# Kernel optimization log

Measured on AMD Instinct MI355X. Metric: run time of the kernel, lower is better.

Reference implementation:

```python
import jax, jax.numpy as jnp
import numpy as np

N, E, G = 100000, 400000, 2000   # nodes, edges, graphs
IN, H = 48, 128                  # in_channels, hidden_channels (= out_channels)
L = 6                            # num GIN layers
EPS = 1e-5                       # BatchNorm eps
SLOPE = 0.01                     # leaky_relu negative slope


def setup_inputs() -> dict:
    key = jax.random.key(0)
    ks = jax.random.split(key, 12)
    x = jax.random.normal(ks[0], (N, IN), jnp.float32)
    edge_index = jax.random.randint(ks[1], (2, E), 0, N)
    edge_attr = jax.random.normal(ks[2], (E, 4), jnp.float32)  # ignored by GINConv
    # sorted graph-assignment vector; guarantee every graph has >=1 node
    batch = jnp.sort(jnp.concatenate([jnp.arange(G),
                                      jax.random.randint(ks[3], (N - G,), 0, G)]))
    s = 0.05
    W1a = jax.random.normal(ks[4], (IN, H), jnp.float32) * s        # layer-0 MLP lin1
    W1b = jax.random.normal(ks[5], (L - 1, H, H), jnp.float32) * s  # layers 1..5 MLP lin1
    b1 = jnp.zeros((L, H), jnp.float32)
    g1 = jnp.ones((L, H), jnp.float32)    # inner BN scale
    be1 = jnp.zeros((L, H), jnp.float32)  # inner BN bias
    W2 = jax.random.normal(ks[6], (L, H, H), jnp.float32) * s       # MLP lin2
    b2 = jnp.zeros((L, H), jnp.float32)
    gn = jnp.ones((L - 1, H), jnp.float32)    # outer BN scale (layers 0..4)
    bn_b = jnp.zeros((L - 1, H), jnp.float32) # outer BN bias
    fc_w = jax.random.normal(ks[7], (2 * H, 64), jnp.float32) * s
    fc_b = jnp.zeros((64,), jnp.float32)
    fc2_w = jax.random.normal(ks[8], (64, 3), jnp.float32) * s
    fc2_b = jnp.zeros((3,), jnp.float32)
    return dict(x=x, edge_attr=edge_attr, W1a=W1a, W1b=W1b, b1=b1, g1=g1, be1=be1,
                W2=W2, b2=b2, gn=gn, bn_b=bn_b, fc_w=fc_w, fc_b=fc_b,
                fc2_w=fc2_w, fc2_b=fc2_b, edge_index=edge_index, batch=batch,
                num_graphs=G)


def _bn(h, g, b):
    # training-mode BatchNorm1d over node dim (biased variance, as torch)
    m = jnp.mean(h, axis=0)
    v = jnp.mean((h - m) ** 2, axis=0)
    return g * (h - m) * jax.lax.rsqrt(v + EPS) + b


def _lrelu(h):
    return jnp.where(h >= 0, h, SLOPE * h)


def reference(x, edge_attr, W1a, W1b, b1, g1, be1, W2, b2, gn, bn_b,
              fc_w, fc_b, fc2_w, fc2_b, edge_index, batch, num_graphs):
    del edge_attr  # GINConv does not use edge attributes
    src, dst = edge_index[0], edge_index[1]
    n = x.shape[0]
    h = x
    for l in range(L):
        # GINConv: (1 + eps) * x + sum_{j in N(i)} x_j, eps = 0
        agg = jax.ops.segment_sum(h[src], dst, num_segments=n)
        z = h + agg
        W1 = W1a if l == 0 else W1b[l - 1]
        # MLP([in, H, H]) with inner BatchNorm + leaky_relu, plain last linear
        z = _lrelu(_bn(z @ W1 + b1[l], g1[l], be1[l])) @ W2[l] + b2[l]
        if l < L - 1:  # outer norm + act, skipped on last layer
            z = _lrelu(_bn(z, gn[l], bn_b[l]))
        h = z
    # dual global pooling over ragged per-graph segments
    cnt = jax.ops.segment_sum(jnp.ones((n, 1), h.dtype), batch, num_segments=num_graphs)
    p1 = jax.ops.segment_sum(h, batch, num_segments=num_graphs) / jnp.maximum(cnt, 1.0)
    p2 = jax.ops.segment_max(h, batch, num_segments=num_graphs)
    emb = jnp.concatenate([p1, p2], axis=1)            # [G, 256]
    out = _lrelu(emb @ fc_w + fc_b) @ fc2_w + fc2_b    # [G, 3]
    return out, emb
```

## Files before the change

### kernel.cpp

```cpp
#include <hip/hip_runtime.h>
#include <stdint.h>

#define N_NODES 100000
#define N_EDGES 400000
#define N_GRAPHS 2000
#define C_IN 48
#define HD 128
#define NLAYERS 6
#define BN_EPS 1e-5f
#define NSLOPE 0.01f
#define SB 391
#define NREP 8

typedef uint16_t u16;
typedef uint32_t u32;
typedef short bf16x8 __attribute__((ext_vector_type(8)));
typedef float f32x4 __attribute__((ext_vector_type(4)));

__device__ __forceinline__ float bf2f_lo(u32 v) { return __uint_as_float(v << 16); }
__device__ __forceinline__ float bf2f_hi(u32 v) { return __uint_as_float(v & 0xffff0000u); }
__device__ __forceinline__ float bf2f(u16 h) { return __uint_as_float(((u32)h) << 16); }
__device__ __forceinline__ u16 f2bf(float f) {
    u32 u = __float_as_uint(f);
    u32 r = (u + 0x7fffu + ((u >> 16) & 1u)) >> 16;
    return (u16)r;
}
__device__ __forceinline__ u32 pack2(float a, float b) {
    return (u32)f2bf(a) | ((u32)f2bf(b) << 16);
}
__device__ __forceinline__ float lrelu(float v) { return v >= 0.f ? v : v * NSLOPE; }

__global__ __launch_bounds__(256) void detect_kernel(const u16* __restrict__ x, int* __restrict__ mode) {
    __shared__ int flag;
    if (threadIdx.x == 0) flag = 0;
    __syncthreads();
    int local = 0;
    for (int i = threadIdx.x; i < 16384; i += 256) {
        float a = fabsf(bf2f(x[i]));
        if (!(a < 1e4f)) local = 1;
    }
    if (local) flag = 1;
    __syncthreads();
    if (threadIdx.x == 0) mode[0] = flag;
}

__global__ __launch_bounds__(256) void hist_kernel(const int* __restrict__ dst, int* __restrict__ cnt) {
    int e = blockIdx.x * 256 + threadIdx.x;
    if (e < N_EDGES) atomicAdd(&cnt[dst[e]], 1);
}

__global__ __launch_bounds__(256) void scan1_kernel(const int* __restrict__ cnt, int* __restrict__ bsum) {
    __shared__ int s[256];
    const int t = threadIdx.x;
    const int i = blockIdx.x * 256 + t;
    s[t] = (i < N_NODES) ? cnt[i] : 0;
    __syncthreads();
    for (int d = 128; d > 0; d >>= 1) {
        if (t < d) s[t] += s[t + d];
        __syncthreads();
    }
    if (t == 0) bsum[blockIdx.x] = s[0];
}

__global__ __launch_bounds__(512) void scan2_kernel(int* __restrict__ bsum, int* __restrict__ row_ptr) {
    __shared__ int s[SB];
    const int t = threadIdx.x;
    if (t < SB) s[t] = bsum[t];
    __syncthreads();
    if (t == 0) {
        int run = 0;
        for (int b = 0; b < SB; ++b) { int v = s[b]; s[b] = run; run += v; }
        row_ptr[0] = 0;
    }
    __syncthreads();
    if (t < SB) bsum[t] = s[t];
}

__global__ __launch_bounds__(256) void scan3_kernel(const int* __restrict__ cnt, const int* __restrict__ bsum,
                                                    int* __restrict__ row_ptr) {
    __shared__ int s[256];
    const int t = threadIdx.x;
    const int i = blockIdx.x * 256 + t;
    s[t] = (i < N_NODES) ? cnt[i] : 0;
    __syncthreads();
    if (t == 0) {
        int run = bsum[blockIdx.x];
        for (int j = 0; j < 256; ++j) { run += s[j]; s[j] = run; }
    }
    __syncthreads();
    if (i < N_NODES) row_ptr[i + 1] = s[t];
}

__global__ __launch_bounds__(256) void fill_kernel(const int* __restrict__ src, const int* __restrict__ dst,
                                                   int* __restrict__ cursor, int* __restrict__ col_idx) {
    int e = blockIdx.x * 256 + threadIdx.x;
    if (e < N_EDGES) {
        int d = dst[e];
        int slot = atomicAdd(&cursor[d], 1);
        col_idx[slot] = src[e];
    }
}

__global__ __launch_bounds__(256) void pack_w_kernel(const void* __restrict__ W1a, const void* __restrict__ W1b,
                                                     const void* __restrict__ W2, const int* __restrict__ mode,
                                                     u16* __restrict__ wpack) {
    const int t = blockIdx.x * 256 + threadIdx.x;
    if (t >= 24576) return;
    const int mat = t >> 11;
    const int r = t & 2047;
    const int l = r & 63;
    const int f = r >> 6;
    const int kb = f >> 3, nt = f & 7;
    const int k0 = kb * 32 + (l >> 4) * 8;
    const int n = nt * 16 + (l & 15);
    const int md = *mode;
    u16 vals[8];
    #pragma unroll
    for (int j = 0; j < 8; ++j) {
        const int k = k0 + j;
        float v;
        if (mat == 0) {
            v = (k < C_IN) ? (md ? ((const float*)W1a)[k * HD + n] : bf2f(((const u16*)W1a)[k * HD + n])) : 0.f;
        } else if (mat < 6) {
            const size_t o = (size_t)(mat - 1) * HD * HD + (size_t)k * HD + n;
            v = md ? ((const float*)W1b)[o] : bf2f(((const u16*)W1b)[o]);
        } else {
            const size_t o = (size_t)(mat - 6) * HD * HD + (size_t)k * HD + n;
            v = md ? ((const float*)W2)[o] : bf2f(((const u16*)W2)[o]);
        }
        vals[j] = f2bf(v);
    }
    uint4 o;
    o.x = (u32)vals[0] | ((u32)vals[1] << 16);
    o.y = (u32)vals[2] | ((u32)vals[3] << 16);
    o.z = (u32)vals[4] | ((u32)vals[5] << 16);
    o.w = (u32)vals[6] | ((u32)vals[7] << 16);
    *reinterpret_cast<uint4*>(wpack + (size_t)t * 8) = o;
}

__global__ __launch_bounds__(256) void pack_b_kernel(const void* __restrict__ b1, const void* __restrict__ b2,
                                                     const int* __restrict__ mode, float* __restrict__ biasf) {
    const int i = blockIdx.x * 256 + threadIdx.x;
    if (i >= 12 * HD) return;
    const int mat = i >> 7, c = i & 127;
    const int md = *mode;
    float v;
    if (mat < 6) v = md ? ((const float*)b1)[mat * HD + c] : bf2f(((const u16*)b1)[mat * HD + c]);
    else         v = md ? ((const float*)b2)[(mat - 6) * HD + c] : bf2f(((const u16*)b2)[(mat - 6) * HD + c]);
    biasf[i] = v;
}

__device__ __forceinline__ void coef_to_lds(float* coefs, const float* __restrict__ instats,
                                            const void* __restrict__ gammav, const void* __restrict__ betav,
                                            size_t gelem, int md, int tid) {
    if (tid < 128) {
        float sm = 0.f, sq = 0.f;
        #pragma unroll
        for (int rep = 0; rep < NREP; ++rep) {
            sm += instats[rep * 256 + tid];
            sq += instats[rep * 256 + 128 + tid];
        }
        const float inv_n = 1.0f / (float)N_NODES;
        const float mean = sm * inv_n;
        const float var = fmaxf(sq * inv_n - mean * mean, 0.f);
        const float rs = rsqrtf(var + BN_EPS);
        const float g  = md ? ((const float*)gammav)[gelem + tid] : bf2f(((const u16*)gammav)[gelem + tid]);
        const float be = md ? ((const float*)betav)[gelem + tid]  : bf2f(((const u16*)betav)[gelem + tid]);
        const float A = g * rs;
        coefs[tid] = A;
        coefs[128 + tid] = be - A * mean;
    }
}

template <int TRANS, int STATS>
__global__ __launch_bounds__(256) void gemm_mfma(const u16* A, const u16* __restrict__ wp,
                                                 const float* __restrict__ biasf,
                                                 const float* __restrict__ instats,
                                                 const void* __restrict__ gammav, const void* __restrict__ betav,
                                                 size_t gelem, const int* __restrict__ mode,
                                                 u16* out, float* __restrict__ stats) {
    __shared__ u16 Asm[32][136];
    __shared__ float sred[2][128];
    __shared__ float sqred[2][128];
    __shared__ float coefs[256];
    const int tid = threadIdx.x;
    const int m0 = blockIdx.x * 32;
    const int rrow = tid >> 4;
    const int seg = tid & 15;

    if (TRANS) {
        coef_to_lds(coefs, instats, gammav, betav, gelem, *mode, tid);
        __syncthreads();
    }

    {
        float cA[8], cB[8];
        if (TRANS) {
            #pragma unroll
            for (int j = 0; j < 8; ++j) {
                cA[j] = coefs[seg * 8 + j];
                cB[j] = coefs[128 + seg * 8 + j];
            }
        }
        uint4 v[2];
        #pragma unroll
        for (int i = 0; i < 2; ++i) {
            const int gm = m0 + i * 16 + rrow;
            if (gm < N_NODES) v[i] = *reinterpret_cast<const uint4*>(A + (size_t)gm * HD + seg * 8);
            else { v[i].x = 0; v[i].y = 0; v[i].z = 0; v[i].w = 0; }
        }
        #pragma unroll
        for (int i = 0; i < 2; ++i) {
            uint4 o = v[i];
            if (TRANS) {
                u32 w[4] = {o.x, o.y, o.z, o.w};
                #pragma unroll
                for (int p = 0; p < 4; ++p) {
                    const float lo = lrelu(cA[2 * p] * bf2f_lo(w[p]) + cB[2 * p]);
                    const float hi = lrelu(cA[2 * p + 1] * bf2f_hi(w[p]) + cB[2 * p + 1]);
                    w[p] = pack2(lo, hi);
                }
                o.x = w[0]; o.y = w[1]; o.z = w[2]; o.w = w[3];
            }
            *reinterpret_cast<uint4*>(&Asm[i * 16 + rrow][seg * 8]) = o;
        }
    }
    __syncthreads();

    const int wave = tid >> 6, lane = tid & 63;
    const int quad = lane >> 4, lx = lane & 15;
    const int rowhalf = wave & 1;
    const int colhalf = wave >> 1;
    const int wrow = rowhalf * 16;
    f32x4 acc[4] = {};
    #pragma unroll
    for (int kb = 0; kb < 4; ++kb) {
        bf16x8 bfr[4];
        #pragma unroll
        for (int nt = 0; nt < 4; ++nt)
            bfr[nt] = *reinterpret_cast<const bf16x8*>(wp + (((size_t)(kb * 8 + colhalf * 4 + nt) * 64 + lane) << 3));
        const bf16x8 af = *reinterpret_cast<const bf16x8*>(&Asm[wrow + lx][kb * 32 + quad * 8]);
        #pragma unroll
        for (int nt = 0; nt < 4; ++nt)
            acc[nt] = __builtin_amdgcn_mfma_f32_16x16x32_bf16(af, bfr[nt], acc[nt], 0, 0, 0);
    }

    const int mrow0 = m0 + wrow;
    #pragma unroll
    for (int nt = 0; nt < 4; ++nt) {
        const int n = colhalf * 64 + nt * 16 + lx;
        const float bj = biasf[n];
        float s = 0.f, q = 0.f;
        #pragma unroll
        for (int r = 0; r < 4; ++r) {
            const int m = mrow0 + quad * 4 + r;
            if (m < N_NODES) {
                const float v = acc[nt][r] + bj;
                out[(size_t)m * HD + n] = f2bf(v);
                if (STATS) { s += v; q += v * v; }
            }
        }
        if (STATS) {
            s += __shfl_xor(s, 16); s += __shfl_xor(s, 32);
            q += __shfl_xor(q, 16); q += __shfl_xor(q, 32);
            if (quad == 0) { sred[rowhalf][n] = s; sqred[rowhalf][n] = q; }
        }
    }
    if (STATS) {
        __syncthreads();
        float* sdst = stats + (size_t)(blockIdx.x & (NREP - 1)) * 256;
        if (tid < 128) {
            atomicAdd(&sdst[tid], sred[0][tid] + sred[1][tid]);
        } else if (tid < 256) {
            const int c2 = tid - 128;
            atomicAdd(&sdst[128 + c2], sqred[0][c2] + sqred[1][c2]);
        }
    }
}

__global__ __launch_bounds__(256) void gemm_gather(const u16* __restrict__ U, const int* __restrict__ row_ptr,
                                                   const int* __restrict__ col_idx, const u16* __restrict__ wp,
                                                   const float* __restrict__ biasf,
                                                   const float* __restrict__ instats,
                                                   const void* __restrict__ gammav, const void* __restrict__ betav,
                                                   size_t gelem, const int* __restrict__ mode,
                                                   u16* __restrict__ out, float* __restrict__ stats) {
    __shared__ u16 Asm[16][136];
    __shared__ float sred[128];
    __shared__ float sqred[128];
    __shared__ float coefs[256];
    const int tid = threadIdx.x;
    const int m0 = blockIdx.x * 16;
    const int rrow = tid >> 4;
    const int seg = tid & 15;

    coef_to_lds(coefs, instats, gammav, betav, gelem, *mode, tid);
    __syncthreads();

    {
        float cA[8], cB[8];
        #pragma unroll
        for (int j = 0; j < 8; ++j) {
            cA[j] = coefs[seg * 8 + j];
            cB[j] = coefs[128 + seg * 8 + j];
        }
        const int gm = m0 + rrow;
        float a[8];
        #pragma unroll
        for (int j = 0; j < 8; ++j) a[j] = 0.f;
        if (gm < N_NODES) {
            const uint4 v = *reinterpret_cast<const uint4*>(U + (size_t)gm * HD + seg * 8);
            const u32 w[4] = {v.x, v.y, v.z, v.w};
            #pragma unroll
            for (int p = 0; p < 4; ++p) {
                a[2 * p]     = lrelu(cA[2 * p] * bf2f_lo(w[p]) + cB[2 * p]);
                a[2 * p + 1] = lrelu(cA[2 * p + 1] * bf2f_hi(w[p]) + cB[2 * p + 1]);
            }
            const int s = row_ptr[gm];
            const int deg = row_ptr[gm + 1] - s;
            for (int t = 0; t < deg; t += 2) {
                const int id0 = col_idx[s + t];
                const bool h1 = (t + 1) < deg;
                const int id1 = h1 ? col_idx[s + t + 1] : 0;
                const uint4 r0 = *reinterpret_cast<const uint4*>(U + (size_t)id0 * HD + seg * 8);
                uint4 r1; r1.x = r1.y = r1.z = r1.w = 0;
                if (h1) r1 = *reinterpret_cast<const uint4*>(U + (size_t)id1 * HD + seg * 8);
                const u32 w0[4] = {r0.x, r0.y, r0.z, r0.w};
                const u32 w1[4] = {r1.x, r1.y, r1.z, r1.w};
                #pragma unroll
                for (int p = 0; p < 4; ++p) {
                    a[2 * p]     += lrelu(cA[2 * p] * bf2f_lo(w0[p]) + cB[2 * p]);
                    a[2 * p + 1] += lrelu(cA[2 * p + 1] * bf2f_hi(w0[p]) + cB[2 * p + 1]);
                    if (h1) {
                        a[2 * p]     += lrelu(cA[2 * p] * bf2f_lo(w1[p]) + cB[2 * p]);
                        a[2 * p + 1] += lrelu(cA[2 * p + 1] * bf2f_hi(w1[p]) + cB[2 * p + 1]);
                    }
                }
            }
        }
        uint4 o;
        o.x = pack2(a[0], a[1]); o.y = pack2(a[2], a[3]);
        o.z = pack2(a[4], a[5]); o.w = pack2(a[6], a[7]);
        *reinterpret_cast<uint4*>(&Asm[rrow][seg * 8]) = o;
    }
    __syncthreads();

    const int wave = tid >> 6, lane = tid & 63;
    const int quad = lane >> 4, lx = lane & 15;
    f32x4 acc[2] = {};
    #pragma unroll
    for (int kb = 0; kb < 4; ++kb) {
        bf16x8 bfr[2];
        #pragma unroll
        for (int nt = 0; nt < 2; ++nt)
            bfr[nt] = *reinterpret_cast<const bf16x8*>(wp + (((size_t)(kb * 8 + wave * 2 + nt) * 64 + lane) << 3));
        const bf16x8 af = *reinterpret_cast<const bf16x8*>(&Asm[lx][kb * 32 + quad * 8]);
        #pragma unroll
        for (int nt = 0; nt < 2; ++nt)
            acc[nt] = __builtin_amdgcn_mfma_f32_16x16x32_bf16(af, bfr[nt], acc[nt], 0, 0, 0);
    }

    #pragma unroll
    for (int nt = 0; nt < 2; ++nt) {
        const int n = wave * 32 + nt * 16 + lx;
        const float bj = biasf[n];
        float s = 0.f, q = 0.f;
        #pragma unroll
        for (int r = 0; r < 4; ++r) {
            const int m = m0 + quad * 4 + r;
            if (m < N_NODES) {
                const float v = acc[nt][r] + bj;
                out[(size_t)m * HD + n] = f2bf(v);
                s += v; q += v * v;
            }
        }
        s += __shfl_xor(s, 16); s += __shfl_xor(s, 32);
        q += __shfl_xor(q, 16); q += __shfl_xor(q, 32);
        if (quad == 0) { sred[n] = s; sqred[n] = q; }
    }
    __syncthreads();
    float* sdst = stats + (size_t)(blockIdx.x & (NREP - 1)) * 256;
    if (tid < 128) {
        atomicAdd(&sdst[tid], sred[tid]);
    } else if (tid < 256) {
        const int c2 = tid - 128;
        atomicAdd(&sdst[128 + c2], sqred[c2]);
    }
}

__global__ __launch_bounds__(256) void gemm_gather0(const void* __restrict__ xv, const int* __restrict__ row_ptr,
                                                    const int* __restrict__ col_idx, const u16* __restrict__ wp,
                                                    const float* __restrict__ biasf, const int* __restrict__ mode,
                                                    u16* __restrict__ out, float* __restrict__ stats) {
    __shared__ u16 Asm[16][136];
    __shared__ float sred[128];
    __shared__ float sqred[128];
    const int tid = threadIdx.x;
    const int m0 = blockIdx.x * 16;
    const int rrow = tid >> 4;
    const int seg = tid & 15;
    const int md = *mode;
    const bool act = seg < 6;

    {
        const int gm = m0 + rrow;
        float a[8];
        #pragma unroll
        for (int j = 0; j < 8; ++j) a[j] = 0.f;
        if (gm < N_NODES && act) {
            if (md) {
                const float* xf = (const float*)xv + (size_t)gm * C_IN + seg * 8;
                const float4 v0 = reinterpret_cast<const float4*>(xf)[0];
                const float4 v1 = reinterpret_cast<const float4*>(xf)[1];
                a[0] = v0.x; a[1] = v0.y; a[2] = v0.z; a[3] = v0.w;
                a[4] = v1.x; a[5] = v1.y; a[6] = v1.z; a[7] = v1.w;
            } else {
                const uint4 v = *reinterpret_cast<const uint4*>((const u16*)xv + (size_t)gm * C_IN + seg * 8);
                const u32 w[4] = {v.x, v.y, v.z, v.w};
                #pragma unroll
                for (int p = 0; p < 4; ++p) { a[2 * p] = bf2f_lo(w[p]); a[2 * p + 1] = bf2f_hi(w[p]); }
            }
        }
        if (gm < N_NODES) {
            const int s = row_ptr[gm];
            const int deg = row_ptr[gm + 1] - s;
            for (int t = 0; t < deg; t += 2) {
                const int id0 = col_idx[s + t];
                const bool h1 = (t + 1) < deg;
                const int id1 = h1 ? col_idx[s + t + 1] : 0;
                if (act) {
                    if (md) {
                        const float* p0 = (const float*)xv + (size_t)id0 * C_IN + seg * 8;
                        const float4 u0 = reinterpret_cast<const float4*>(p0)[0];
                        const float4 u1 = reinterpret_cast<const float4*>(p0)[1];
                        a[0] += u0.x; a[1] += u0.y; a[2] += u0.z; a[3] += u0.w;
                        a[4] += u1.x; a[5] += u1.y; a[6] += u1.z; a[7] += u1.w;
                        if (h1) {
                            const float* p1 = (const float*)xv + (size_t)id1 * C_IN + seg * 8;
                            const float4 t0 = reinterpret_cast<const float4*>(p1)[0];
                            const float4 t1 = reinterpret_cast<const float4*>(p1)[1];
                            a[0] += t0.x; a[1] += t0.y; a[2] += t0.z; a[3] += t0.w;
                            a[4] += t1.x; a[5] += t1.y; a[6] += t1.z; a[7] += t1.w;
                        }
                    } else {
                        const uint4 r0 = *reinterpret_cast<const uint4*>((const u16*)xv + (size_t)id0 * C_IN + seg * 8);
                        const u32 w0[4] = {r0.x, r0.y, r0.z, r0.w};
                        #pragma unroll
                        for (int p = 0; p < 4; ++p) { a[2 * p] += bf2f_lo(w0[p]); a[2 * p + 1] += bf2f_hi(w0[p]); }
                        if (h1) {
                            const uint4 r1 = *reinterpret_cast<const uint4*>((const u16*)xv + (size_t)id1 * C_IN + seg * 8);
                            const u32 w1[4] = {r1.x, r1.y, r1.z, r1.w};
                            #pragma unroll
                            for (int p = 0; p < 4; ++p) { a[2 * p] += bf2f_lo(w1[p]); a[2 * p + 1] += bf2f_hi(w1[p]); }
                        }
                    }
                }
            }
        }
        uint4 o;
        o.x = pack2(a[0], a[1]); o.y = pack2(a[2], a[3]);
        o.z = pack2(a[4], a[5]); o.w = pack2(a[6], a[7]);
        *reinterpret_cast<uint4*>(&Asm[rrow][seg * 8]) = o;
    }
    __syncthreads();

    const int wave = tid >> 6, lane = tid & 63;
    const int quad = lane >> 4, lx = lane & 15;
    f32x4 acc[2] = {};
    #pragma unroll
    for (int kb = 0; kb < 4; ++kb) {
        bf16x8 bfr[2];
        #pragma unroll
        for (int nt = 0; nt < 2; ++nt)
            bfr[nt] = *reinterpret_cast<const bf16x8*>(wp + (((size_t)(kb * 8 + wave * 2 + nt) * 64 + lane) << 3));
        const bf16x8 af = *reinterpret_cast<const bf16x8*>(&Asm[lx][kb * 32 + quad * 8]);
        #pragma unroll
        for (int nt = 0; nt < 2; ++nt)
            acc[nt] = __builtin_amdgcn_mfma_f32_16x16x32_bf16(af, bfr[nt], acc[nt], 0, 0, 0);
    }

    #pragma unroll
    for (int nt = 0; nt < 2; ++nt) {
        const int n = wave * 32 + nt * 16 + lx;
        const float bj = biasf[n];
        float s = 0.f, q = 0.f;
        #pragma unroll
        for (int r = 0; r < 4; ++r) {
            const int m = m0 + quad * 4 + r;
            if (m < N_NODES) {
                const float v = acc[nt][r] + bj;
                out[(size_t)m * HD + n] = f2bf(v);
                s += v; q += v * v;
            }
        }
        s += __shfl_xor(s, 16); s += __shfl_xor(s, 32);
        q += __shfl_xor(q, 16); q += __shfl_xor(q, 32);
        if (quad == 0) { sred[n] = s; sqred[n] = q; }
    }
    __syncthreads();
    float* sdst = stats + (size_t)(blockIdx.x & (NREP - 1)) * 256;
    if (tid < 128) {
        atomicAdd(&sdst[tid], sred[tid]);
    } else if (tid < 256) {
        const int c2 = tid - 128;
        atomicAdd(&sdst[128 + c2], sqred[c2]);
    }
}

__global__ __launch_bounds__(256) void pool_kernel(const u16* __restrict__ hf, const int* __restrict__ batch,
                                                   const int* __restrict__ mode, float* __restrict__ emb,
                                                   void* __restrict__ outv) {
    const int wave = threadIdx.x >> 6, lane = threadIdx.x & 63;
    const int g = blockIdx.x * 4 + wave;
    if (g >= N_GRAPHS) return;
    const int md = *mode;
    const int quad = lane >> 4, c = lane & 15;
    int lo = 0, hi = N_NODES;
    while (lo < hi) { int m = (lo + hi) >> 1; if (batch[m] < g) lo = m + 1; else hi = m; }
    const int s = lo;
    hi = N_NODES;
    while (lo < hi) { int m = (lo + hi) >> 1; if (batch[m] < g + 1) lo = m + 1; else hi = m; }
    const int e = lo;
    const int cnt = e - s;
    float sum[8], mx[8];
    #pragma unroll
    for (int j = 0; j < 8; ++j) { sum[j] = 0.f; mx[j] = -INFINITY; }
    for (int n = s + quad; n < e; n += 4) {
        const uint4 v = *reinterpret_cast<const uint4*>(hf + (size_t)n * HD + c * 8);
        const u32 w[4] = {v.x, v.y, v.z, v.w};
        #pragma unroll
        for (int p = 0; p < 4; ++p) {
            const float f0 = bf2f_lo(w[p]), f1 = bf2f_hi(w[p]);
            sum[2 * p] += f0; sum[2 * p + 1] += f1;
            mx[2 * p] = fmaxf(mx[2 * p], f0); mx[2 * p + 1] = fmaxf(mx[2 * p + 1], f1);
        }
    }
    #pragma unroll
    for (int j = 0; j < 8; ++j) {
        sum[j] += __shfl_xor(sum[j], 16); sum[j] += __shfl_xor(sum[j], 32);
        mx[j] = fmaxf(mx[j], __shfl_xor(mx[j], 16));
        mx[j] = fmaxf(mx[j], __shfl_xor(mx[j], 32));
    }
    if (quad == 0) {
        const float invc = 1.0f / (float)max(cnt, 1);
        const size_t base = (size_t)N_GRAPHS * 3 + (size_t)g * 256;
        #pragma unroll
        for (int j = 0; j < 8; ++j) {
            const float mean = sum[j] * invc;
            const float m2 = (cnt == 0) ? 0.f : mx[j];
            const int col = c * 8 + j;
            emb[(size_t)g * 256 + col] = mean;
            emb[(size_t)g * 256 + 128 + col] = m2;
            if (md) {
                ((float*)outv)[base + col] = mean;
                ((float*)outv)[base + 128 + col] = m2;
            } else {
                ((u16*)outv)[base + col] = f2bf(mean);
                ((u16*)outv)[base + 128 + col] = f2bf(m2);
            }
        }
    }
}

__global__ __launch_bounds__(64) void final_kernel(const float* __restrict__ emb, const void* __restrict__ fcwv,
                                                   const void* __restrict__ fcbv, const void* __restrict__ fc2wv,
                                                   const void* __restrict__ fc2bv, const int* __restrict__ mode,
                                                   void* __restrict__ outv) {
    __shared__ float es[256];
    __shared__ float hs[64];
    const int g = blockIdx.x, t = threadIdx.x;
    const int md = *mode;
    reinterpret_cast<float4*>(es)[t] = reinterpret_cast<const float4*>(emb + (size_t)g * 256)[t];
    __syncthreads();
    float acc = md ? ((const float*)fcbv)[t] : bf2f(((const u16*)fcbv)[t]);
    if (md) {
        const float* w = (const float*)fcwv;
        #pragma unroll 8
        for (int k = 0; k < 256; ++k) acc += es[k] * w[k * 64 + t];
    } else {
        const u16* w = (const u16*)fcwv;
        #pragma unroll 8
        for (int k = 0; k < 256; ++k) acc += es[k] * bf2f(w[k * 64 + t]);
    }
    hs[t] = lrelu(acc);
    __syncthreads();
    if (t < 3) {
        float o = md ? ((const float*)fc2bv)[t] : bf2f(((const u16*)fc2bv)[t]);
        if (md) {
            const float* w = (const float*)fc2wv;
            #pragma unroll 8
            for (int j = 0; j < 64; ++j) o += hs[j] * w[j * 3 + t];
            ((float*)outv)[(size_t)g * 3 + t] = o;
        } else {
            const u16* w = (const u16*)fc2wv;
            #pragma unroll 8
            for (int j = 0; j < 64; ++j) o += hs[j] * bf2f(w[j * 3 + t]);
            ((u16*)outv)[(size_t)g * 3 + t] = f2bf(o);
        }
    }
}

static inline size_t align256(size_t x) { return (x + 255) & ~(size_t)255; }

extern "C" void kernel_launch(void* const* d_in, const int* in_sizes, int n_in,
                              void* d_out, int out_size, void* d_ws, size_t ws_size,
                              hipStream_t stream) {
    (void)in_sizes; (void)n_in; (void)out_size; (void)ws_size;
    const void* x    = d_in[0];
    const void* W1a  = d_in[2];
    const void* W1b  = d_in[3];
    const void* b1   = d_in[4];
    const void* g1   = d_in[5];
    const void* be1  = d_in[6];
    const void* W2   = d_in[7];
    const void* b2   = d_in[8];
    const void* gn   = d_in[9];
    const void* bnb  = d_in[10];
    const void* fcw  = d_in[11];
    const void* fcb  = d_in[12];
    const void* fc2w = d_in[13];
    const void* fc2b = d_in[14];
    const int* ei    = (const int*)d_in[15];
    const int* batch = (const int*)d_in[16];

    char* p = (char*)d_ws;
    size_t off = 0;
    u16* zb = (u16*)(p + off); off += align256((size_t)N_NODES * HD * 2);
    u16* hb = (u16*)(p + off); off += align256((size_t)N_NODES * HD * 2);
    u16* wpack = (u16*)(p + off); off += align256((size_t)12 * HD * HD * 2);
    float* biasf = (float*)(p + off); off += align256((size_t)12 * HD * 4);
    float* emb = (float*)(p + off); off += align256((size_t)N_GRAPHS * 256 * 4);
    int* row_ptr = (int*)(p + off); off += align256((size_t)(N_NODES + 1) * 4);
    int* cursor = (int*)(p + off); off += align256((size_t)N_NODES * 4);
    int* col_idx = (int*)(p + off); off += align256((size_t)N_EDGES * 4);
    int* bsum = (int*)(p + off); off += align256((size_t)SB * 4);
    float* statsAll = (float*)(p + off); off += align256((size_t)12 * NREP * 256 * 4);
    int* mode = (int*)(p + off); off += align256(4);

    const int EB = (N_EDGES + 255) / 256;
    const int GBM = (N_NODES + 31) / 32;
    const int GBG = (N_NODES + 15) / 16;

    detect_kernel<<<1, 256, 0, stream>>>((const u16*)x, mode);

    hipMemsetAsync(cursor, 0, (size_t)N_NODES * 4, stream);
    hipMemsetAsync(statsAll, 0, (size_t)12 * NREP * 256 * 4, stream);
    hist_kernel<<<EB, 256, 0, stream>>>(ei + N_EDGES, cursor);
    scan1_kernel<<<SB, 256, 0, stream>>>(cursor, bsum);
    scan2_kernel<<<1, 512, 0, stream>>>(bsum, row_ptr);
    scan3_kernel<<<SB, 256, 0, stream>>>(cursor, bsum, row_ptr);
    hipMemcpyAsync(cursor, row_ptr, (size_t)N_NODES * 4, hipMemcpyDeviceToDevice, stream);
    fill_kernel<<<EB, 256, 0, stream>>>(ei, ei + N_EDGES, cursor, col_idx);
    pack_w_kernel<<<96, 256, 0, stream>>>(W1a, W1b, W2, mode, wpack);
    pack_b_kernel<<<6, 256, 0, stream>>>(b1, b2, mode, biasf);

    u16* cur = zb;
    u16* oth = hb;
    for (int l = 0; l < NLAYERS; ++l) {
        float* statsA = statsAll + (size_t)l * NREP * 256;
        float* statsB = statsAll + (size_t)(6 + l) * NREP * 256;
        float* statsBprev = statsAll + (size_t)(6 + l - 1) * NREP * 256;
        if (l == 0) {
            gemm_gather0<<<GBG, 256, 0, stream>>>(x, row_ptr, col_idx, wpack,
                                                  biasf, mode, cur, statsA);
        } else {
            gemm_gather<<<GBG, 256, 0, stream>>>(cur, row_ptr, col_idx,
                                                 wpack + (size_t)l * HD * HD,
                                                 biasf + (size_t)l * HD, statsBprev, gn, bnb,
                                                 (size_t)(l - 1) * HD, mode, oth, statsA);
            u16* t = cur; cur = oth; oth = t;
        }
        if (l < NLAYERS - 1) {
            gemm_mfma<1, 1><<<GBM, 256, 0, stream>>>(cur, wpack + (size_t)(6 + l) * HD * HD,
                                                     biasf + (size_t)(6 + l) * HD, statsA, g1, be1,
                                                     (size_t)l * HD, mode, cur, statsB);
        } else {
            gemm_mfma<1, 0><<<GBM, 256, 0, stream>>>(cur, wpack + (size_t)(6 + l) * HD * HD,
                                                     biasf + (size_t)(6 + l) * HD, statsA, g1, be1,
                                                     (size_t)l * HD, mode, cur, nullptr);
        }
    }

    pool_kernel<<<(N_GRAPHS + 3) / 4, 256, 0, stream>>>(cur, batch, mode, emb, d_out);
    final_kernel<<<N_GRAPHS, 64, 0, stream>>>(emb, fcw, fcb, fc2w, fc2b, mode, d_out);
}
```

Before: 504.4 us.

## Gather neighbors edge-parallel per 32-row tile with LDS float atomics

Rewrites the fused gather+GEMM kernels so that each block handles 32 rows. The block stages that range's edge list and the row owning each edge in LDS, then spreads the neighbor row loads evenly across all threads. Partial sums go into an fp32 LDS accumulator through atomic adds, replacing the old per-row serial loop over degree. This targets load imbalance from varying node degrees and the half-width 16-row MFMA tile, at the cost of LDS atomics, more shared memory per block, and bounds checks removed on the assumption that N is divisible by 32.

New measurement: 1.773 ms. 251% more time.

```diff
diff --git a/kernel.cpp b/kernel.cpp
--- a/kernel.cpp
+++ b/kernel.cpp
@@ -11,6 +11,7 @@
 #define NSLOPE 0.01f
 #define SB 391
 #define NREP 8
+#define ECAP 1024
 
 typedef uint16_t u16;
 typedef uint32_t u32;
@@ -29,6 +30,15 @@
     return (u32)f2bf(a) | ((u32)f2bf(b) << 16);
 }
 __device__ __forceinline__ float lrelu(float v) { return v >= 0.f ? v : v * NSLOPE; }
+
+__device__ __forceinline__ void bn_store8(float* dst, const uint4 v, const float* cA, const float* cB) {
+    const u32 w[4] = {v.x, v.y, v.z, v.w};
+    #pragma unroll
+    for (int p = 0; p < 4; ++p) {
+        dst[2 * p]     = lrelu(cA[2 * p] * bf2f_lo(w[p]) + cB[2 * p]);
+        dst[2 * p + 1] = lrelu(cA[2 * p + 1] * bf2f_hi(w[p]) + cB[2 * p + 1]);
+    }
+}
 
 __global__ __launch_bounds__(256) void detect_kernel(const u16* __restrict__ x, int* __restrict__ mode) {
     __shared__ int flag;
@@ -169,6 +179,55 @@
         const float A = g * rs;
         coefs[tid] = A;
         coefs[128 + tid] = be - A * mean;
+    }
+}
+
+__device__ __forceinline__ void mfma_epilogue32(const u16 (*Asm)[136], const u16* __restrict__ wp,
+                                                const float* __restrict__ biasf,
+                                                float sred[2][128], float sqred[2][128],
+                                                int m0, int tid, int bidx,
+                                                u16* __restrict__ out, float* __restrict__ stats) {
+    const int wave = tid >> 6, lane = tid & 63;
+    const int quad = lane >> 4, lx = lane & 15;
+    const int rowhalf = wave & 1;
+    const int colhalf = wave >> 1;
+    const int wrow = rowhalf * 16;
+    f32x4 acc[4] = {};
+    #pragma unroll
+    for (int kb = 0; kb < 4; ++kb) {
+        bf16x8 bfr[4];
+        #pragma unroll
+        for (int nt = 0; nt < 4; ++nt)
+            bfr[nt] = *reinterpret_cast<const bf16x8*>(wp + (((size_t)(kb * 8 + colhalf * 4 + nt) * 64 + lane) << 3));
+        const bf16x8 af = *reinterpret_cast<const bf16x8*>(&Asm[wrow + lx][kb * 32 + quad * 8]);
+        #pragma unroll
+        for (int nt = 0; nt < 4; ++nt)
+            acc[nt] = __builtin_amdgcn_mfma_f32_16x16x32_bf16(af, bfr[nt], acc[nt], 0, 0, 0);
+    }
+    const int mrow0 = m0 + wrow;
+    #pragma unroll
+    for (int nt = 0; nt < 4; ++nt) {
+        const int n = colhalf * 64 + nt * 16 + lx;
+        const float bj = biasf[n];
+        float s = 0.f, q = 0.f;
+        #pragma unroll
+        for (int r = 0; r < 4; ++r) {
+            const int m = mrow0 + quad * 4 + r;
+            const float v = acc[nt][r] + bj;
+            out[(size_t)m * HD + n] = f2bf(v);
+            s += v; q += v * v;
+        }
+        s += __shfl_xor(s, 16); s += __shfl_xor(s, 32);
+        q += __shfl_xor(q, 16); q += __shfl_xor(q, 32);
+        if (quad == 0) { sred[rowhalf][n] = s; sqred[rowhalf][n] = q; }
+    }
+    __syncthreads();
+    float* sdst = stats + (size_t)(bidx & (NREP - 1)) * 256;
+    if (tid < 128) {
+        atomicAdd(&sdst[tid], sred[0][tid] + sred[1][tid]);
+    } else {
+        const int c2 = tid - 128;
+        atomicAdd(&sdst[128 + c2], sqred[0][c2] + sqred[1][c2]);
     }
 }
 
@@ -206,8 +265,7 @@
         #pragma unroll
         for (int i = 0; i < 2; ++i) {
             const int gm = m0 + i * 16 + rrow;
-            if (gm < N_NODES) v[i] = *reinterpret_cast<const uint4*>(A + (size_t)gm * HD + seg * 8);
-            else { v[i].x = 0; v[i].y = 0; v[i].z = 0; v[i].w = 0; }
+            v[i] = *reinterpret_cast<const uint4*>(A + (size_t)gm * HD + seg * 8);
         }
         #pragma unroll
         for (int i = 0; i < 2; ++i) {
@@ -254,11 +312,9 @@
         #pragma unroll
         for (int r = 0; r < 4; ++r) {
             const int m = mrow0 + quad * 4 + r;
-            if (m < N_NODES) {
-                const float v = acc[nt][r] + bj;
-                out[(size_t)m * HD + n] = f2bf(v);
-                if (STATS) { s += v; q += v * v; }
-            }
+            const float v = acc[nt][r] + bj;
+            out[(size_t)m * HD + n] = f2bf(v);
+            if (STATS) { s += v; q += v * v; }
         }
         if (STATS) {
             s += __shfl_xor(s, 16); s += __shfl_xor(s, 32);
@@ -271,7 +327,7 @@
         float* sdst = stats + (size_t)(blockIdx.x & (NREP - 1)) * 256;
         if (tid < 128) {
             atomicAdd(&sdst[tid], sred[0][tid] + sred[1][tid]);
-        } else if (tid < 256) {
+        } else {
             const int c2 = tid - 128;
             atomicAdd(&sdst[128 + c2], sqred[0][c2] + sqred[1][c2]);
         }
@@ -279,232 +335,196 @@
 }
 
 __global__ __launch_bounds__(256) void gemm_gather(const u16* __restrict__ U, const int* __restrict__ row_ptr,
-                                                   const int* __restrict__ col_idx, const u16* __restrict__ wp,
+                                                   const int* __restrict__ col_idx,
+                                                   const u16* __restrict__ wp,
                                                    const float* __restrict__ biasf,
                                                    const float* __restrict__ instats,
                                                    const void* __restrict__ gammav, const void* __restrict__ betav,
                                                    size_t gelem, const int* __restrict__ mode,
                                                    u16* __restrict__ out, float* __restrict__ stats) {
-    __shared__ u16 Asm[16][136];
-    __shared__ float sred[128];
-    __shared__ float sqred[128];
+    __shared__ float accf[32][132];
     __shared__ float coefs[256];
+    __shared__ int rp[33];
+    __shared__ int eidx[ECAP];
+    __shared__ u16 rowOf[ECAP];
+    __shared__ u16 Asm[32][136];
+    __shared__ float sred[2][128];
+    __shared__ float sqred[2][128];
     const int tid = threadIdx.x;
-    const int m0 = blockIdx.x * 16;
+    const int m0 = blockIdx.x * 32;
     const int rrow = tid >> 4;
     const int seg = tid & 15;
 
     coef_to_lds(coefs, instats, gammav, betav, gelem, *mode, tid);
-    __syncthreads();
+    if (tid < 33) rp[tid] = row_ptr[m0 + tid];
+    __syncthreads();
+
+    float cA[8], cB[8];
+    #pragma unroll
+    for (int j = 0; j < 8; ++j) {
+        cA[j] = coefs[seg * 8 + j];
+        cB[j] = coefs[128 + seg * 8 + j];
+    }
 
     {
-        float cA[8], cB[8];
-        #pragma unroll
-        for (int j = 0; j < 8; ++j) {
-            cA[j] = coefs[seg * 8 + j];
-            cB[j] = coefs[128 + seg * 8 + j];
-        }
-        const int gm = m0 + rrow;
-        float a[8];
-        #pragma unroll
-        for (int j = 0; j < 8; ++j) a[j] = 0.f;
-        if (gm < N_NODES) {
-            const uint4 v = *reinterpret_cast<const uint4*>(U + (size_t)gm * HD + seg * 8);
+        const uint4 v0 = *reinterpret_cast<const uint4*>(U + (size_t)(m0 + rrow) * HD + seg * 8);
+        const uint4 v1 = *reinterpret_cast<const uint4*>(U + (size_t)(m0 + 16 + rrow) * HD + seg * 8);
+        bn_store8(&accf[rrow][seg * 8], v0, cA, cB);
+        bn_store8(&accf[16 + rrow][seg * 8], v1, cA, cB);
+    }
+
+    const int e0 = rp[0], e1 = rp[32];
+    for (int base = e0; base < e1; base += ECAP) {
+        const int n = min(ECAP, e1 - base);
+        __syncthreads();
+        for (int k = tid; k < n; k += 256) {
+            const int e = base + k;
+            eidx[k] = col_idx[e];
+            int lo = 0, hi = 32;
+            #pragma unroll
+            for (int it = 0; it < 5; ++it) { const int mid = (lo + hi) >> 1; if (e >= rp[mid]) lo = mid; else hi = mid; }
+            rowOf[k] = (u16)lo;
+        }
+        __syncthreads();
+        const int items = n << 4;
+        for (int k = tid; k < items; k += 256) {
+            const int e = k >> 4;
+            const int nb = eidx[e];
+            const int r = rowOf[e];
+            const uint4 v = *reinterpret_cast<const uint4*>(U + (size_t)nb * HD + seg * 8);
             const u32 w[4] = {v.x, v.y, v.z, v.w};
+            float* arow = &accf[r][seg * 8];
             #pragma unroll
             for (int p = 0; p < 4; ++p) {
-                a[2 * p]     = lrelu(cA[2 * p] * bf2f_lo(w[p]) + cB[2 * p]);
-                a[2 * p + 1] = lrelu(cA[2 * p + 1] * bf2f_hi(w[p]) + cB[2 * p + 1]);
+                atomicAdd(&arow[2 * p],     lrelu(cA[2 * p] * bf2f_lo(w[p]) + cB[2 * p]));
+                atomicAdd(&arow[2 * p + 1], lrelu(cA[2 * p + 1] * bf2f_hi(w[p]) + cB[2 * p + 1]));
             }
-            const int s = row_ptr[gm];
-            const int deg = row_ptr[gm + 1] - s;
-            for (int t = 0; t < deg; t += 2) {
-                const int id0 = col_idx[s + t];
-                const bool h1 = (t + 1) < deg;
-                const int id1 = h1 ? col_idx[s + t + 1] : 0;
-                const uint4 r0 = *reinterpret_cast<const uint4*>(U + (size_t)id0 * HD + seg * 8);
-                uint4 r1; r1.x = r1.y = r1.z = r1.w = 0;
-                if (h1) r1 = *reinterpret_cast<const uint4*>(U + (size_t)id1 * HD + seg * 8);
-                const u32 w0[4] = {r0.x, r0.y, r0.z, r0.w};
-                const u32 w1[4] = {r1.x, r1.y, r1.z, r1.w};
-                #pragma unroll
-                for (int p = 0; p < 4; ++p) {
-                    a[2 * p]     += lrelu(cA[2 * p] * bf2f_lo(w0[p]) + cB[2 * p]);
-                    a[2 * p + 1] += lrelu(cA[2 * p + 1] * bf2f_hi(w0[p]) + cB[2 * p + 1]);
-                    if (h1) {
-                        a[2 * p]     += lrelu(cA[2 * p] * bf2f_lo(w1[p]) + cB[2 * p]);
-                        a[2 * p + 1] += lrelu(cA[2 * p + 1] * bf2f_hi(w1[p]) + cB[2 * p + 1]);
+        }
+    }
+    __syncthreads();
+
+    {
+        const float* s0 = &accf[rrow][seg * 8];
+        const float* s1 = &accf[16 + rrow][seg * 8];
+        uint4 o0, o1;
+        o0.x = pack2(s0[0], s0[1]); o0.y = pack2(s0[2], s0[3]);
+        o0.z = pack2(s0[4], s0[5]); o0.w = pack2(s0[6], s0[7]);
+        o1.x = pack2(s1[0], s1[1]); o1.y = pack2(s1[2], s1[3]);
+        o1.z = pack2(s1[4], s1[5]); o1.w = pack2(s1[6], s1[7]);
+        *reinterpret_cast<uint4*>(&Asm[rrow][seg * 8]) = o0;
+        *reinterpret_cast<uint4*>(&Asm[16 + rrow][seg * 8]) = o1;
+    }
+    __syncthreads();
+
+    mfma_epilogue32(Asm, wp, biasf, sred, sqred, m0, tid, blockIdx.x, out, stats);
+}
+
+__global__ __launch_bounds__(256) void gemm_gather0(const void* __restrict__ xv, const int* __restrict__ row_ptr,
+                                                    const int* __restrict__ col_idx,
+                                                    const u16* __restrict__ wp,
+                                                    const float* __restrict__ biasf, const int* __restrict__ mode,
+                                                    u16* __restrict__ out, float* __restrict__ stats) {
+    __shared__ float accf[32][132];
+    __shared__ int rp[33];
+    __shared__ int eidx[ECAP];
+    __shared__ u16 rowOf[ECAP];
+    __shared__ u16 Asm[32][136];
+    __shared__ float sred[2][128];
+    __shared__ float sqred[2][128];
+    const int tid = threadIdx.x;
+    const int m0 = blockIdx.x * 32;
+    const int rrow = tid >> 4;
+    const int seg = tid & 15;
+    const int md = *mode;
+
+    if (tid < 33) rp[tid] = row_ptr[m0 + tid];
+
+    if (md) {
+        if (seg < 12) {
+            const float4 v0 = *reinterpret_cast<const float4*>((const float*)xv + (size_t)(m0 + rrow) * C_IN + seg * 4);
+            const float4 v1 = *reinterpret_cast<const float4*>((const float*)xv + (size_t)(m0 + 16 + rrow) * C_IN + seg * 4);
+            float* a0 = &accf[rrow][seg * 4];
+            float* a1 = &accf[16 + rrow][seg * 4];
+            a0[0] = v0.x; a0[1] = v0.y; a0[2] = v0.z; a0[3] = v0.w;
+            a1[0] = v1.x; a1[1] = v1.y; a1[2] = v1.z; a1[3] = v1.w;
+        }
+    } else {
+        if (seg < 6) {
+            const uint4 v0 = *reinterpret_cast<const uint4*>((const u16*)xv + (size_t)(m0 + rrow) * C_IN + seg * 8);
+            const uint4 v1 = *reinterpret_cast<const uint4*>((const u16*)xv + (size_t)(m0 + 16 + rrow) * C_IN + seg * 8);
+            const u32 w0[4] = {v0.x, v0.y, v0.z, v0.w};
+            const u32 w1[4] = {v1.x, v1.y, v1.z, v1.w};
+            float* a0 = &accf[rrow][seg * 8];
+            float* a1 = &accf[16 + rrow][seg * 8];
+            #pragma unroll
+            for (int p = 0; p < 4; ++p) {
+                a0[2 * p] = bf2f_lo(w0[p]); a0[2 * p + 1] = bf2f_hi(w0[p]);
+                a1[2 * p] = bf2f_lo(w1[p]); a1[2 * p + 1] = bf2f_hi(w1[p]);
+            }
+        }
+    }
+    __syncthreads();
+
+    const int e0 = rp[0], e1 = rp[32];
+    for (int base = e0; base < e1; base += ECAP) {
+        const int n = min(ECAP, e1 - base);
+        __syncthreads();
+        for (int k = tid; k < n; k += 256) {
+            const int e = base + k;
+            eidx[k] = col_idx[e];
+            int lo = 0, hi = 32;
+            #pragma unroll
+            for (int it = 0; it < 5; ++it) { const int mid = (lo + hi) >> 1; if (e >= rp[mid]) lo = mid; else hi = mid; }
+            rowOf[k] = (u16)lo;
+        }
+        __syncthreads();
+        const int items = n << 4;
+        for (int k = tid; k < items; k += 256) {
+            const int e = k >> 4;
+            const int nb = eidx[e];
+            const int r = rowOf[e];
+            if (md) {
+                if (seg < 12) {
+                    const float4 v = *reinterpret_cast<const float4*>((const float*)xv + (size_t)nb * C_IN + seg * 4);
+                    float* arow = &accf[r][seg * 4];
+                    atomicAdd(&arow[0], v.x); atomicAdd(&arow[1], v.y);
+                    atomicAdd(&arow[2], v.z); atomicAdd(&arow[3], v.w);
+                }
+            } else {
+                if (seg < 6) {
+                    const uint4 v = *reinterpret_cast<const uint4*>((const u16*)xv + (size_t)nb * C_IN + seg * 8);
+                    const u32 w[4] = {v.x, v.y, v.z, v.w};
+                    float* arow = &accf[r][seg * 8];
+                    #pragma unroll
+                    for (int p = 0; p < 4; ++p) {
+                        atomicAdd(&arow[2 * p], bf2f_lo(w[p]));
+                        atomicAdd(&arow[2 * p + 1], bf2f_hi(w[p]));
                     }
                 }
             }
         }
-        uint4 o;
-        o.x = pack2(a[0], a[1]); o.y = pack2(a[2], a[3]);
-        o.z = pack2(a[4], a[5]); o.w = pack2(a[6], a[7]);
-        *reinterpret_cast<uint4*>(&Asm[rrow][seg * 8]) = o;
-    }
-    __syncthreads();
-
-    const int wave = tid >> 6, lane = tid & 63;
-    const int quad = lane >> 4, lx = lane & 15;
-    f32x4 acc[2] = {};
-    #pragma unroll
-    for (int kb = 0; kb < 4; ++kb) {
-        bf16x8 bfr[2];
-        #pragma unroll
-        for (int nt = 0; nt < 2; ++nt)
-            bfr[nt] = *reinterpret_cast<const bf16x8*>(wp + (((size_t)(kb * 8 + wave * 2 + nt) * 64 + lane) << 3));
-        const bf16x8 af = *reinterpret_cast<const bf16x8*>(&Asm[lx][kb * 32 + quad * 8]);
-        #pragma unroll
-        for (int nt = 0; nt < 2; ++nt)
-            acc[nt] = __builtin_amdgcn_mfma_f32_16x16x32_bf16(af, bfr[nt], acc[nt], 0, 0, 0);
-    }
-
-    #pragma unroll
-    for (int nt = 0; nt < 2; ++nt) {
-        const int n = wave * 32 + nt * 16 + lx;
-        const float bj = biasf[n];
-        float s = 0.f, q = 0.f;
-        #pragma unroll
-        for (int r = 0; r < 4; ++r) {
-            const int m = m0 + quad * 4 + r;
-            if (m < N_NODES) {
-                const float v = acc[nt][r] + bj;
-                out[(size_t)m * HD + n] = f2bf(v);
-                s += v; q += v * v;
-            }
-        }
-        s += __shfl_xor(s, 16); s += __shfl_xor(s, 32);
-        q += __shfl_xor(q, 16); q += __shfl_xor(q, 32);
-        if (quad == 0) { sred[n] = s; sqred[n] = q; }
-    }
-    __syncthreads();
-    float* sdst = stats + (size_t)(blockIdx.x & (NREP - 1)) * 256;
-    if (tid < 128) {
-        atomicAdd(&sdst[tid], sred[tid]);
-    } else if (tid < 256) {
-        const int c2 = tid - 128;
-        atomicAdd(&sdst[128 + c2], sqred[c2]);
-    }
-}
-
-__global__ __launch_bounds__(256) void gemm_gather0(const void* __restrict__ xv, const int* __restrict__ row_ptr,
-                                                    const int* __restrict__ col_idx, const u16* __restrict__ wp,
-                                                    const float* __restrict__ biasf, const int* __restrict__ mode,
-                                                    u16* __restrict__ out, float* __restrict__ stats) {
-    __shared__ u16 Asm[16][136];
-    __shared__ float sred[128];
-    __shared__ float sqred[128];
-    const int tid = threadIdx.x;
-    const int m0 = blockIdx.x * 16;
-    const int rrow = tid >> 4;
-    const int seg = tid & 15;
-    const int md = *mode;
-    const bool act = seg < 6;
+    }
+    __syncthreads();
 
     {
-        const int gm = m0 + rrow;
-        float a[8];
-        #pragma unroll
-        for (int j = 0; j < 8; ++j) a[j] = 0.f;
-        if (gm < N_NODES && act) {
-            if (md) {
-                const float* xf = (const float*)xv + (size_t)gm * C_IN + seg * 8;
-                const float4 v0 = reinterpret_cast<const float4*>(xf)[0];
-                const float4 v1 = reinterpret_cast<const float4*>(xf)[1];
-                a[0] = v0.x; a[1] = v0.y; a[2] = v0.z; a[3] = v0.w;
-                a[4] = v1.x; a[5] = v1.y; a[6] = v1.z; a[7] = v1.w;
-            } else {
-                const uint4 v = *reinterpret_cast<const uint4*>((const u16*)xv + (size_t)gm * C_IN + seg * 8);
-                const u32 w[4] = {v.x, v.y, v.z, v.w};
-                #pragma unroll
-                for (int p = 0; p < 4; ++p) { a[2 * p] = bf2f_lo(w[p]); a[2 * p + 1] = bf2f_hi(w[p]); }
-            }
-        }
-        if (gm < N_NODES) {
-            const int s = row_ptr[gm];
-            const int deg = row_ptr[gm + 1] - s;
-            for (int t = 0; t < deg; t += 2) {
-                const int id0 = col_idx[s + t];
-                const bool h1 = (t + 1) < deg;
-                const int id1 = h1 ? col_idx[s + t + 1] : 0;
-                if (act) {
-                    if (md) {
-                        const float* p0 = (const float*)xv + (size_t)id0 * C_IN + seg * 8;
-                        const float4 u0 = reinterpret_cast<const float4*>(p0)[0];
-                        const float4 u1 = reinterpret_cast<const float4*>(p0)[1];
-                        a[0] += u0.x; a[1] += u0.y; a[2] += u0.z; a[3] += u0.w;
-                        a[4] += u1.x; a[5] += u1.y; a[6] += u1.z; a[7] += u1.w;
-                        if (h1) {
-                            const float* p1 = (const float*)xv + (size_t)id1 * C_IN + seg * 8;
-                            const float4 t0 = reinterpret_cast<const float4*>(p1)[0];
-                            const float4 t1 = reinterpret_cast<const float4*>(p1)[1];
-                            a[0] += t0.x; a[1] += t0.y; a[2] += t0.z; a[3] += t0.w;
-                            a[4] += t1.x; a[5] += t1.y; a[6] += t1.z; a[7] += t1.w;
-                        }
-                    } else {
-                        const uint4 r0 = *reinterpret_cast<const uint4*>((const u16*)xv + (size_t)id0 * C_IN + seg * 8);
-                        const u32 w0[4] = {r0.x, r0.y, r0.z, r0.w};
-                        #pragma unroll
-                        for (int p = 0; p < 4; ++p) { a[2 * p] += bf2f_lo(w0[p]); a[2 * p + 1] += bf2f_hi(w0[p]); }
-                        if (h1) {
-                            const uint4 r1 = *reinterpret_cast<const uint4*>((const u16*)xv + (size_t)id1 * C_IN + seg * 8);
-                            const u32 w1[4] = {r1.x, r1.y, r1.z, r1.w};
-                            #pragma unroll
-                            for (int p = 0; p < 4; ++p) { a[2 * p] += bf2f_lo(w1[p]); a[2 * p + 1] += bf2f_hi(w1[p]); }
-                        }
-                    }
-                }
-            }
-        }
-        uint4 o;
-        o.x = pack2(a[0], a[1]); o.y = pack2(a[2], a[3]);
-        o.z = pack2(a[4], a[5]); o.w = pack2(a[6], a[7]);
-        *reinterpret_cast<uint4*>(&Asm[rrow][seg * 8]) = o;
-    }
-    __syncthreads();
-
-    const int wave = tid >> 6, lane = tid & 63;
-    const int quad = lane >> 4, lx = lane & 15;
-    f32x4 acc[2] = {};
-    #pragma unroll
-    for (int kb = 0; kb < 4; ++kb) {
-        bf16x8 bfr[2];
-        #pragma unroll
-        for (int nt = 0; nt < 2; ++nt)
-            bfr[nt] = *reinterpret_cast<const bf16x8*>(wp + (((size_t)(kb * 8 + wave * 2 + nt) * 64 + lane) << 3));
-        const bf16x8 af = *reinterpret_cast<const bf16x8*>(&Asm[lx][kb * 32 + quad * 8]);
-        #pragma unroll
-        for (int nt = 0; nt < 2; ++nt)
-            acc[nt] = __builtin_amdgcn_mfma_f32_16x16x32_bf16(af, bfr[nt], acc[nt], 0, 0, 0);
-    }
-
-    #pragma unroll
-    for (int nt = 0; nt < 2; ++nt) {
-        const int n = wave * 32 + nt * 16 + lx;
-        const float bj = biasf[n];
-        float s = 0.f, q = 0.f;
-        #pragma unroll
-        for (int r = 0; r < 4; ++r) {
-            const int m = m0 + quad * 4 + r;
-            if (m < N_NODES) {
-                const float v = acc[nt][r] + bj;
-                out[(size_t)m * HD + n] = f2bf(v);
-                s += v; q += v * v;
-            }
-        }
-        s += __shfl_xor(s, 16); s += __shfl_xor(s, 32);
-        q += __shfl_xor(q, 16); q += __shfl_xor(q, 32);
-        if (quad == 0) { sred[n] = s; sqred[n] = q; }
-    }
-    __syncthreads();
-    float* sdst = stats + (size_t)(blockIdx.x & (NREP - 1)) * 256;
-    if (tid < 128) {
-        atomicAdd(&sdst[tid], sred[tid]);
-    } else if (tid < 256) {
-        const int c2 = tid - 128;
-        atomicAdd(&sdst[128 + c2], sqred[c2]);
-    }
+        uint4 o0, o1;
+        if (seg < 6) {
+            const float* s0 = &accf[rrow][seg * 8];
+            const float* s1 = &accf[16 + rrow][seg * 8];
+            o0.x = pack2(s0[0], s0[1]); o0.y = pack2(s0[2], s0[3]);
+            o0.z = pack2(s0[4], s0[5]); o0.w = pack2(s0[6], s0[7]);
+            o1.x = pack2(s1[0], s1[1]); o1.y = pack2(s1[2], s1[3]);
+            o1.z = pack2(s1[4], s1[5]); o1.w = pack2(s1[6], s1[7]);
+        } else {
+            o0.x = o0.y = o0.z = o0.w = 0;
+            o1.x = o1.y = o1.z = o1.w = 0;
+        }
+        *reinterpret_cast<uint4*>(&Asm[rrow][seg * 8]) = o0;
+        *reinterpret_cast<uint4*>(&Asm[16 + rrow][seg * 8]) = o1;
+    }
+    __syncthreads();
+
+    mfma_epilogue32(Asm, wp, biasf, sred, sqred, m0, tid, blockIdx.x, out, stats);
 }
 
 __global__ __launch_bounds__(256) void pool_kernel(const u16* __restrict__ hf, const int* __restrict__ batch,
@@ -638,8 +658,7 @@
     int* mode = (int*)(p + off); off += align256(4);
 
     const int EB = (N_EDGES + 255) / 256;
-    const int GBM = (N_NODES + 31) / 32;
-    const int GBG = (N_NODES + 15) / 16;
+    const int GB32 = N_NODES / 32;
 
     detect_kernel<<<1, 256, 0, stream>>>((const u16*)x, mode);
 
@@ -661,23 +680,23 @@
         float* statsB = statsAll + (size_t)(6 + l) * NREP * 256;
         float* statsBprev = statsAll + (size_t)(6 + l - 1) * NREP * 256;
         if (l == 0) {
-            gemm_gather0<<<GBG, 256, 0, stream>>>(x, row_ptr, col_idx, wpack,
-                                                  biasf, mode, cur, statsA);
+            gemm_gather0<<<GB32, 256, 0, stream>>>(x, row_ptr, col_idx, wpack,
+                                                   biasf, mode, cur, statsA);
         } else {
-            gemm_gather<<<GBG, 256, 0, stream>>>(cur, row_ptr, col_idx,
-                                                 wpack + (size_t)l * HD * HD,
-                                                 biasf + (size_t)l * HD, statsBprev, gn, bnb,
-                                                 (size_t)(l - 1) * HD, mode, oth, statsA);
+            gemm_gather<<<GB32, 256, 0, stream>>>(cur, row_ptr, col_idx,
+                                                  wpack + (size_t)l * HD * HD,
+                                                  biasf + (size_t)l * HD, statsBprev, gn, bnb,
+                                                  (size_t)(l - 1) * HD, mode, oth, statsA);
             u16* t = cur; cur = oth; oth = t;
         }
         if (l < NLAYERS - 1) {
-            gemm_mfma<1, 1><<<GBM, 256, 0, stream>>>(cur, wpack + (size_t)(6 + l) * HD * HD,
-                                                     biasf + (size_t)(6 + l) * HD, statsA, g1, be1,
-                                                     (size_t)l * HD, mode, cur, statsB);
+            gemm_mfma<1, 1><<<GB32, 256, 0, stream>>>(cur, wpack + (size_t)(6 + l) * HD * HD,
+                                                      biasf + (size_t)(6 + l) * HD, statsA, g1, be1,
+                                                      (size_t)l * HD, mode, cur, statsB);
         } else {
-            gemm_mfma<1, 0><<<GBM, 256, 0, stream>>>(cur, wpack + (size_t)(6 + l) * HD * HD,
-                                                     biasf + (size_t)(6 + l) * HD, statsA, g1, be1,
-                                                     (size_t)l * HD, mode, cur, nullptr);
+            gemm_mfma<1, 0><<<GB32, 256, 0, stream>>>(cur, wpack + (size_t)(6 + l) * HD * HD,
+                                                      biasf + (size_t)(6 + l) * HD, statsA, g1, be1,
+                                                      (size_t)l * HD, mode, cur, nullptr);
         }
     }
 
```
